# Performance work log

Measured on AMD Instinct MI355X. Metric: run time of the kernel, lower is better.

The kernel has to match this reference:

```python
import jax, jax.numpy as jnp
import numpy as np

N = 50000
E = 1600000
D_IN = 128
D_OUT = 128
K_EIG = 4
N_AGG = 3
N_SCALE = 3
AVG_D_LOG = float(np.log(33.0))  # avg_d['log'] for avg degree 32
BN_EPS = 1e-5


def setup_inputs() -> dict:
    key = jax.random.key(0)
    ks = jax.random.split(key, 8)
    h = jax.random.normal(ks[0], (N, D_IN), dtype=jnp.float32)
    eig = jax.random.normal(ks[1], (N, K_EIG), dtype=jnp.float32)
    snorm_n = jax.random.uniform(ks[2], (N, 1), dtype=jnp.float32)
    edge_src = jax.random.randint(ks[3], (E,), 0, N, dtype=jnp.int32)
    edge_dst = jax.random.randint(ks[4], (E,), 0, N, dtype=jnp.int32)
    d_cat = N_AGG * N_SCALE * D_IN  # 1152
    W = jax.random.normal(ks[5], (d_cat, D_OUT), dtype=jnp.float32) / np.sqrt(d_cat)
    b = jnp.zeros((D_OUT,), dtype=jnp.float32)
    bn_gamma = jnp.ones((D_OUT,), dtype=jnp.float32)
    bn_beta = jnp.zeros((D_OUT,), dtype=jnp.float32)
    bn_mean = jax.random.normal(ks[6], (D_OUT,), dtype=jnp.float32) * 0.1
    bn_var = jnp.ones((D_OUT,), dtype=jnp.float32)
    return {"h": h, "eig": eig, "snorm_n": snorm_n, "W": W, "b": b,
            "bn_gamma": bn_gamma, "bn_beta": bn_beta, "bn_mean": bn_mean,
            "bn_var": bn_var, "edge_src": edge_src, "edge_dst": edge_dst}


def reference(h, eig, snorm_n, W, b, bn_gamma, bn_beta, bn_mean, bn_var, edge_src, edge_dst):
    h_in = h
    # --- pretrans_edges: message e = src h; vector_field = eig_src - eig_dst ---
    h_e = h[edge_src]                      # [E, d] gathered edge messages
    vf = eig[edge_src] - eig[edge_dst]     # [E, k_eig]
    w = jnp.abs(vf[:, 0:1])                # dir1 weights [E, 1]

    # --- reduce: multi-aggregator segment reduce over destination nodes ---
    deg = jax.ops.segment_sum(jnp.ones((E,), h.dtype), edge_dst, num_segments=N)  # [N]
    deg_safe = jnp.maximum(deg, 1.0)
    sum_h = jax.ops.segment_sum(h_e, edge_dst, num_segments=N)
    mean_h = sum_h / deg_safe[:, None]
    max_h = jax.ops.segment_max(h_e, edge_dst, num_segments=N)
    max_h = jnp.where(deg[:, None] > 0, max_h, 0.0)  # empty mailbox -> 0
    dir_num = jax.ops.segment_sum(h_e * w, edge_dst, num_segments=N)
    dir_den = jax.ops.segment_sum(w, edge_dst, num_segments=N)  # [N, 1]
    dir_av = dir_num / (dir_den + 1e-30)
    agg = jnp.concatenate([mean_h, max_h, dir_av], axis=1)  # [N, 3d]

    # --- scalers: identity, amplification, attenuation ---
    logD = jnp.log(deg + 1.0)[:, None]
    amp = agg * (logD / AVG_D_LOG)
    att = agg * (AVG_D_LOG / jnp.maximum(logD, 1e-6))
    hcat = jnp.concatenate([agg, amp, att], axis=1)  # [N, 9d]

    # --- posttrans MLP (1 layer, no activation) ---
    out = hcat @ W + b
    # graph norm
    out = out * snorm_n
    # batch norm (eval mode, running stats)
    out = (out - bn_mean) * jax.lax.rsqrt(bn_var + BN_EPS) * bn_gamma + bn_beta
    out = jax.nn.relu(out)
    # residual (in_dim == out_dim)
    out = h_in + out
    # dropout p=0.0 / eval -> identity
    return out
```

## Files before the change

kernel.cpp:

```cpp
#include <hip/hip_runtime.h>
#include <hip/hip_bf16.h>

#define DIN 128
#define KEIG 4
#define CAP 96
#define BSH 7
#define BCAP 5120
#define ITEMS 16
#define AVG_D_LOG 3.4965075614664802f
#define BN_EPS 1e-5f

typedef __attribute__((ext_vector_type(8))) short bf16x8;
typedef __attribute__((ext_vector_type(4))) float f32x4;
typedef __attribute__((ext_vector_type(2))) float f32x2;

static __device__ inline unsigned short f2bf(float f) {
    union { float f; unsigned u; } v; v.f = f;
    unsigned r = v.u + 0x7FFFu + ((v.u >> 16) & 1u);
    return (unsigned short)(r >> 16);
}
static __device__ inline unsigned pack2bf(float lo, float hi) {
    return (unsigned)f2bf(lo) | ((unsigned)f2bf(hi) << 16);
}
static __device__ inline f32x2 up2(unsigned u) {
    f32x2 r;
    r.x = __int_as_float(u << 16);
    r.y = __int_as_float(u & 0xffff0000u);
    return r;
}


__global__ void k_prep(const float* __restrict__ h, unsigned* __restrict__ hb,
                       const float* __restrict__ W, unsigned short* __restrict__ Wt,
                       const float* __restrict__ eig, float* __restrict__ eig0,
                       int* __restrict__ cursor, int* __restrict__ bcur,
                       int nPairs, int wTotal, int N, int nbk)
{
    int i = blockIdx.x * 256 + threadIdx.x;
    if (i < nPairs) {
        float2 v = reinterpret_cast<const float2*>(h)[i];
        hb[i] = pack2bf(v.x, v.y);
    }
    if (i < wTotal) {
        int k = i % 384;
        int rest = i / 384;
        int col = rest & 127;
        int s = rest >> 7;
        Wt[i] = f2bf(W[(s * 384 + k) * 128 + col]);
    }
    if (i < N) {
        eig0[i] = eig[(size_t)i * KEIG];
        cursor[i] = 0;
    }
    if (i < nbk) bcur[i] = 0;
}


__global__ void k_bucket(const int* __restrict__ src, const int* __restrict__ dst,
                         const float* __restrict__ eig0, int* __restrict__ bcur,
                         uint2* __restrict__ stag, int E, int nbk)
{
    __shared__ int lcnt[512];
    __shared__ int lbase[512];
    const int t = threadIdx.x;
    for (int b = t; b < nbk; b += 256) lcnt[b] = 0;
    __syncthreads();

    const int e0 = blockIdx.x * (256 * ITEMS);
    int   bky[ITEMS];
    int   rnk[ITEMS];
    uint2 rec[ITEMS];
#pragma unroll
    for (int k = 0; k < ITEMS; ++k) {
        const int e = e0 + t + k * 256;
        if (e < E) {
            const int s = src[e], d = dst[e];
            const float w = fabsf(eig0[s] - eig0[d]);
            rec[k] = make_uint2(((unsigned)f2bf(w) << 16) | (unsigned)s, (unsigned)d);
            bky[k] = d >> BSH;
            rnk[k] = atomicAdd(&lcnt[bky[k]], 1);
        } else bky[k] = -1;
    }
    __syncthreads();
    for (int b = t; b < nbk; b += 256) {
        const int c = lcnt[b];
        lbase[b] = c ? atomicAdd(&bcur[b], c) : 0;
    }
    __syncthreads();
#pragma unroll
    for (int k = 0; k < ITEMS; ++k) {
        if (bky[k] >= 0) {
            const int pos = lbase[bky[k]] + rnk[k];
            if (pos < BCAP) stag[(size_t)bky[k] * BCAP + pos] = rec[k];
        }
    }
}


__global__ void k_group(const int* __restrict__ bcur, const uint2* __restrict__ stag,
                        unsigned* __restrict__ final_, int* __restrict__ off,
                        int* __restrict__ cnt, int N)
{
    __shared__ uint2 sst[BCAP];
    __shared__ int hcnt[128];
    __shared__ int sbuf[2][128];
    const int b = blockIdx.x;
    const int t = threadIdx.x;
    const int cb = min(bcur[b], BCAP);

    for (int i = t; i < cb; i += 256) sst[i] = stag[(size_t)b * BCAP + i];
    if (t < 128) hcnt[t] = 0;
    __syncthreads();

    int dl[(BCAP + 255) / 256];
    int rk[(BCAP + 255) / 256];
    int nit = 0;
    for (int i = t; i < cb; i += 256) {
        const int d_loc = sst[i].y & 127;
        dl[nit] = d_loc;
        rk[nit] = atomicAdd(&hcnt[d_loc], 1);
        ++nit;
    }
    __syncthreads();

    int cur = 0;
    if (t < 128) sbuf[0][t] = hcnt[t];
    __syncthreads();
    for (int d = 1; d < 128; d <<= 1) {
        if (t < 128) {
            int x = sbuf[cur][t];
            if (t >= d) x += sbuf[cur][t - d];
            sbuf[cur ^ 1][t] = x;
        }
        cur ^= 1;
        __syncthreads();
    }
    const int exb = cur ^ 1;
    if (t < 128) sbuf[exb][t] = sbuf[cur][t] - hcnt[t];
    __syncthreads();

    if (t < 128) {
        const int dg = (b << BSH) + t;
        if (dg < N) {
            off[dg] = b * BCAP + sbuf[exb][t];
            cnt[dg] = hcnt[t];
        }
    }
    nit = 0;
    for (int i = t; i < cb; i += 256) {
        final_[(size_t)b * BCAP + sbuf[exb][dl[nit]] + rk[nit]] = sst[i].x;
        ++nit;
    }
}


__global__ void k_hist(const int* __restrict__ dst, int* __restrict__ counts, int E) {
    int e = blockIdx.x * 256 + threadIdx.x;
    if (e < E) atomicAdd(&counts[dst[e]], 1);
}

__global__ void k_part(const int* __restrict__ counts, int* __restrict__ part, int N) {
    __shared__ int red[4];
    const int t = threadIdx.x;
    const int i = blockIdx.x * 256 + t;
    int v = (i < N) ? counts[i] : 0;
    for (int d = 32; d >= 1; d >>= 1) v += __shfl_down(v, d, 64);
    if ((t & 63) == 0) red[t >> 6] = v;
    __syncthreads();
    if (t == 0) part[blockIdx.x] = red[0] + red[1] + red[2] + red[3];
}

__global__ void k_scan1(const int* __restrict__ part, int* __restrict__ partoff,
                        int* __restrict__ total_out, int NB) {
    __shared__ int buf[2][256];
    const int t = threadIdx.x;
    int v = (t < NB) ? part[t] : 0;
    buf[0][t] = v;
    __syncthreads();
    int cur = 0;
    for (int d = 1; d < 256; d <<= 1) {
        int x = buf[cur][t];
        if (t >= d) x += buf[cur][t - d];
        buf[cur ^ 1][t] = x;
        cur ^= 1;
        __syncthreads();
    }
    if (t < NB) partoff[t] = buf[cur][t] - v;
    if (t == 255) *total_out = buf[cur][255];
}

__global__ void k_off(const int* __restrict__ counts, const int* __restrict__ partoff,
                      int* __restrict__ offsets, int* __restrict__ cursor, int N) {
    __shared__ int buf[2][256];
    const int t = threadIdx.x;
    const int i = blockIdx.x * 256 + t;
    int v = (i < N) ? counts[i] : 0;
    buf[0][t] = v;
    __syncthreads();
    int cur = 0;
    for (int d = 1; d < 256; d <<= 1) {
        int x = buf[cur][t];
        if (t >= d) x += buf[cur][t - d];
        buf[cur ^ 1][t] = x;
        cur ^= 1;
        __syncthreads();
    }
    if (i < N) {
        int excl = partoff[blockIdx.x] + buf[cur][t] - v;
        offsets[i] = excl;
        cursor[i]  = excl;
    }
}

__global__ void k_fill_csr(const int* __restrict__ src, const int* __restrict__ dst,
                           const float* __restrict__ eig0, int* __restrict__ cursor,
                           int2* __restrict__ sedge, int E)
{
    int e = blockIdx.x * 256 + threadIdx.x;
    if (e < E) {
        int s = src[e], d = dst[e];
        float w = fabsf(eig0[s] - eig0[d]);
        int pos = atomicAdd(&cursor[d], 1);
        sedge[pos] = make_int2(s, __float_as_int(w));
    }
}


template<bool PACKED>
__launch_bounds__(256, 3)
__global__ void k_aggmm(const unsigned* __restrict__ hb, const float* __restrict__ h,
                        const float* __restrict__ snorm,
                        const float* __restrict__ bvec, const float* __restrict__ gam,
                        const float* __restrict__ bet, const float* __restrict__ bmean,
                        const float* __restrict__ bvar,
                        const int* __restrict__ idx0, const int* __restrict__ idx1,
                        const unsigned* __restrict__ upk, const int2* __restrict__ sedge,
                        const unsigned short* __restrict__ Wt,
                        float* __restrict__ out, int N)
{
    __shared__ unsigned short aggT[32][392];
    __shared__ unsigned slotbuf[32][CAP];
    __shared__ float sc1[32], sc2[32];

    const int tid  = threadIdx.x;
    const int wave = tid >> 6;
    const int lane = tid & 63;
    const int q    = lane >> 4;
    const int l16  = lane & 15;
    const int node0 = blockIdx.x * 32;

    const uint4* __restrict__ hb4 = reinterpret_cast<const uint4*>(hb);

    for (int i = 0; i < 2; ++i) {
        const int nl = wave * 8 + i * 4 + q;
        const int n  = node0 + nl;
        int e0 = 0, cnt = 0;
        if (n < N) {
            if (PACKED) { e0 = idx0[n]; cnt = min(idx1[n], CAP); }
            else        { e0 = idx0[n]; cnt = idx0[n + 1] - e0; }
        }
        const int c0 = __shfl(cnt, 0),  c1 = __shfl(cnt, 16);
        const int c2 = __shfl(cnt, 32), c3 = __shfl(cnt, 48);
        const int maxcnt = max(max(c0, c1), max(c2, c3));

        f32x2 s2[4], m2[4], d2[4];
        float wsum = 0.f;
#pragma unroll
        for (int f = 0; f < 4; ++f) {
            s2[f] = (f32x2){0.f, 0.f};
            m2[f] = (f32x2){-INFINITY, -INFINITY};
            d2[f] = (f32x2){0.f, 0.f};
        }
        const int clampi = (cnt > 0) ? cnt - 1 : 0;

        if (PACKED) {
            for (int t = l16; t < cnt; t += 16) slotbuf[nl][t] = upk[e0 + t];
            if (cnt == 0 && l16 == 0) slotbuf[nl][0] = 0;

            uint4 bufA[8], bufB[8];
            float wvA[8], wvB[8];

#define STAGE(BUF, WV, BASE) do {                                        \
    _Pragma("unroll")                                                    \
    for (int j = 0; j < 8; ++j) {                                        \
        int ci = (BASE) + j; ci = ci < clampi ? ci : clampi;             \
        const unsigned u = slotbuf[nl][ci];                              \
        WV[j] = __int_as_float(u & 0xffff0000u);                         \
        BUF[j] = hb4[(((u & 0xffffu) << 4) | (unsigned)l16)];            \
    }                                                                    \
} while (0)

#define ACCUM(BUF, WV, BASE) do {                                        \
    _Pragma("unroll")                                                    \
    for (int j = 0; j < 8; ++j) {                                        \
        if ((BASE) + j < cnt) {                                          \
            const float wj = WV[j];                                      \
            const f32x2 wj2 = (f32x2){wj, wj};                           \
            const f32x2 p0 = up2(BUF[j].x), p1 = up2(BUF[j].y);          \
            const f32x2 p2 = up2(BUF[j].z), p3 = up2(BUF[j].w);          \
            s2[0] += p0; s2[1] += p1; s2[2] += p2; s2[3] += p3;          \
            m2[0].x = fmaxf(m2[0].x, p0.x); m2[0].y = fmaxf(m2[0].y, p0.y); \
            m2[1].x = fmaxf(m2[1].x, p1.x); m2[1].y = fmaxf(m2[1].y, p1.y); \
            m2[2].x = fmaxf(m2[2].x, p2.x); m2[2].y = fmaxf(m2[2].y, p2.y); \
            m2[3].x = fmaxf(m2[3].x, p3.x); m2[3].y = fmaxf(m2[3].y, p3.y); \
            d2[0] += p0 * wj2; d2[1] += p1 * wj2;                        \
            d2[2] += p2 * wj2; d2[3] += p3 * wj2;                        \
            wsum += wj;                                                  \
        }                                                                \
    }                                                                    \
} while (0)

            if (maxcnt > 0) {
                STAGE(bufA, wvA, 0);
                for (int base = 0; base < maxcnt; base += 16) {
                    const bool haveB = (base + 8) < maxcnt;
                    if (haveB) STAGE(bufB, wvB, base + 8);
                    ACCUM(bufA, wvA, base);
                    if (base + 16 < maxcnt) STAGE(bufA, wvA, base + 16);
                    if (haveB) ACCUM(bufB, wvB, base + 8);
                }
            }
#undef STAGE
#undef ACCUM
        } else {
            for (int base = 0; base < maxcnt; base += 8) {
                unsigned srcs[8];
                float    wv[8];
#pragma unroll
                for (int j = 0; j < 8; ++j) {
                    int idx = base + j;
                    idx = idx < clampi ? idx : clampi;
                    int2 v = sedge[e0 + idx];
                    srcs[j] = (unsigned)((cnt > 0) ? v.x : 0);
                    wv[j]   = __int_as_float(v.y);
                }
                uint4 v8[8];
#pragma unroll
                for (int j = 0; j < 8; ++j)
                    v8[j] = hb4[(size_t)srcs[j] * 16 + l16];
#pragma unroll
                for (int j = 0; j < 8; ++j) {
                    if (base + j < cnt) {
                        const float wj = wv[j];
                        const f32x2 wj2 = (f32x2){wj, wj};
                        const f32x2 p0 = up2(v8[j].x), p1 = up2(v8[j].y);
                        const f32x2 p2 = up2(v8[j].z), p3 = up2(v8[j].w);
                        s2[0] += p0; s2[1] += p1; s2[2] += p2; s2[3] += p3;
                        m2[0].x = fmaxf(m2[0].x, p0.x); m2[0].y = fmaxf(m2[0].y, p0.y);
                        m2[1].x = fmaxf(m2[1].x, p1.x); m2[1].y = fmaxf(m2[1].y, p1.y);
                        m2[2].x = fmaxf(m2[2].x, p2.x); m2[2].y = fmaxf(m2[2].y, p2.y);
                        m2[3].x = fmaxf(m2[3].x, p3.x); m2[3].y = fmaxf(m2[3].y, p3.y);
                        d2[0] += p0 * wj2; d2[1] += p1 * wj2;
                        d2[2] += p2 * wj2; d2[3] += p3 * wj2;
                        wsum += wj;
                    }
                }
            }
        }

        const float degf = (float)cnt;
        const float inv  = 1.0f / fmaxf(degf, 1.0f);
        const float dinv = 1.0f / (wsum + 1e-30f);
        const bool nz = (cnt > 0);
        uint4 pm, px, pd;
        pm.x = pack2bf(s2[0].x * inv, s2[0].y * inv);
        pm.y = pack2bf(s2[1].x * inv, s2[1].y * inv);
        pm.z = pack2bf(s2[2].x * inv, s2[2].y * inv);
        pm.w = pack2bf(s2[3].x * inv, s2[3].y * inv);
        px.x = pack2bf(nz ? m2[0].x : 0.f, nz ? m2[0].y : 0.f);
        px.y = pack2bf(nz ? m2[1].x : 0.f, nz ? m2[1].y : 0.f);
        px.z = pack2bf(nz ? m2[2].x : 0.f, nz ? m2[2].y : 0.f);
        px.w = pack2bf(nz ? m2[3].x : 0.f, nz ? m2[3].y : 0.f);
        pd.x = pack2bf(d2[0].x * dinv, d2[0].y * dinv);
        pd.y = pack2bf(d2[1].x * dinv, d2[1].y * dinv);
        pd.z = pack2bf(d2[2].x * dinv, d2[2].y * dinv);
        pd.w = pack2bf(d2[3].x * dinv, d2[3].y * dinv);
        const int f0i = l16 * 8;
        *reinterpret_cast<uint4*>(&aggT[nl][f0i])       = pm;
        *reinterpret_cast<uint4*>(&aggT[nl][128 + f0i]) = px;
        *reinterpret_cast<uint4*>(&aggT[nl][256 + f0i]) = pd;
        if (l16 == 0) {
            float logD = logf(degf + 1.0f);
            sc1[nl] = logD / AVG_D_LOG;
            sc2[nl] = AVG_D_LOG / fmaxf(logD, 1e-6f);
        }
    }
    __syncthreads();

    f32x4 acc[2][2][3];
#pragma unroll
    for (int m = 0; m < 2; ++m)
#pragma unroll
        for (int ct = 0; ct < 2; ++ct)
#pragma unroll
            for (int sv = 0; sv < 3; ++sv)
                acc[m][ct][sv] = (f32x4){0.f, 0.f, 0.f, 0.f};

    const int cb   = wave * 32;
    const int r16  = lane & 15;
    const int kgrp = lane >> 4;

    for (int ks = 0; ks < 12; ++ks) {
        const int kbase = ks * 32 + kgrp * 8;
        bf16x8 a[2];
#pragma unroll
        for (int m = 0; m < 2; ++m)
            a[m] = *reinterpret_cast<const bf16x8*>(&aggT[m * 16 + r16][kbase]);
#pragma unroll
        for (int sv = 0; sv < 3; ++sv) {
#pragma unroll
            for (int ct = 0; ct < 2; ++ct) {
                const int col = cb + ct * 16 + r16;
                const bf16x8 b = *reinterpret_cast<const bf16x8*>(
                    &Wt[(size_t)sv * 49152 + (size_t)col * 384 + kbase]);
#pragma unroll
                for (int m = 0; m < 2; ++m)
                    acc[m][ct][sv] = __builtin_amdgcn_mfma_f32_16x16x32_bf16(
                        a[m], b, acc[m][ct][sv], 0, 0, 0);
            }
        }
    }

#pragma unroll
    for (int ct = 0; ct < 2; ++ct) {
        const int col = cb + ct * 16 + r16;
        const float bc  = bvec[col];
        const float mc  = bmean[col];
        const float rs  = rsqrtf(bvar[col] + BN_EPS);
        const float gc  = gam[col];
        const float bec = bet[col];
#pragma unroll
        for (int m = 0; m < 2; ++m) {
#pragma unroll
            for (int r = 0; r < 4; ++r) {
                const int nl = m * 16 + kgrp * 4 + r;
                const int n  = node0 + nl;
                if (n >= N) continue;
                float v = acc[m][ct][0][r] + sc1[nl] * acc[m][ct][1][r]
                                           + sc2[nl] * acc[m][ct][2][r];
                float y = (v + bc) * snorm[n];
                y = (y - mc) * rs * gc + bec;
                y = fmaxf(y, 0.f);
                y += h[(size_t)n * DIN + col];
                out[(size_t)n * DIN + col] = y;
            }
        }
    }
}


extern "C" void kernel_launch(void* const* d_in, const int* in_sizes, int n_in,
                              void* d_out, int out_size, void* d_ws, size_t ws_size,
                              hipStream_t stream)
{
    const float* h     = (const float*)d_in[0];
    const float* eig   = (const float*)d_in[1];
    const float* snorm = (const float*)d_in[2];
    const float* W     = (const float*)d_in[3];
    const float* bvec  = (const float*)d_in[4];
    const float* gam   = (const float*)d_in[5];
    const float* bet   = (const float*)d_in[6];
    const float* bmean = (const float*)d_in[7];
    const float* bvar  = (const float*)d_in[8];
    const int*   esrc  = (const int*)d_in[9];
    const int*   edst  = (const int*)d_in[10];
    float* out = (float*)d_out;

    const int N = in_sizes[0] / DIN;
    const int E = in_sizes[9];
    const int NB = (N + 255) / 256;
    const int nPairs = N * DIN / 2;
    const int wTotal = 3 * 128 * 384;
    const int nbk = (N + 127) >> BSH;
    (void)ws_size; (void)n_in; (void)out_size;

    char* base = (char*)d_ws;
    size_t o = 0;
    auto take = [&](size_t bytes) {
        char* p = base + o;
        o = (o + bytes + 255) & ~(size_t)255;
        return p;
    };
    unsigned* hb       = (unsigned*)take((size_t)nPairs * 4);
    unsigned short* Wt = (unsigned short*)take((size_t)wTotal * 2);
    float* eig0        = (float*)take((size_t)N * 4);
    int* cursor        = (int*)take((size_t)(N + 1) * 4);

    const size_t bucket_bytes = (size_t)nbk * BCAP * 8
                              + (size_t)nbk * BCAP * 4
                              + (size_t)N * 8
                              + (size_t)nbk * 4 + 4096;
    const bool bucketOK = (N <= 65536) && (nbk <= 512) && ((o + bucket_bytes) <= ws_size);

    const int gridPrep = (nPairs + 255) / 256;
    const int gridE    = (E + 255) / 256;
    const int gridB    = (E + 256 * ITEMS - 1) / (256 * ITEMS);
    const int gridN32  = (N + 31) / 32;

    if (bucketOK) {
        uint2* stag     = (uint2*)take((size_t)nbk * BCAP * 8);
        unsigned* fin   = (unsigned*)take((size_t)nbk * BCAP * 4);
        int* off        = (int*)take((size_t)N * 4);
        int* cnt        = (int*)take((size_t)N * 4);
        int* bcur       = (int*)take((size_t)nbk * 4);
        k_prep<<<gridPrep, 256, 0, stream>>>(h, hb, W, Wt, eig, eig0, cursor, bcur,
                                             nPairs, wTotal, N, nbk);
        k_bucket<<<gridB, 256, 0, stream>>>(esrc, edst, eig0, bcur, stag, E, nbk);
        k_group<<<nbk, 256, 0, stream>>>(bcur, stag, fin, off, cnt, N);
        k_aggmm<true><<<gridN32, 256, 0, stream>>>(hb, h, snorm, bvec, gam, bet, bmean,
                                                   bvar, off, cnt, fin, nullptr, Wt, out, N);
    } else {
        int* counts  = (int*)take((size_t)(N + 1) * 4);
        int* offsets = (int*)take((size_t)(N + 1) * 4);
        int2* sedge  = (int2*)take((size_t)(E + 16) * 8);
        int* part    = (int*)take((size_t)NB * 4);
        int* partoff = (int*)take((size_t)NB * 4);
        int* bcur    = (int*)take(4096);
        k_prep<<<gridPrep, 256, 0, stream>>>(h, hb, W, Wt, eig, eig0, counts, bcur,
                                             nPairs, wTotal, N, 1);
        k_hist<<<gridE, 256, 0, stream>>>(edst, counts, E);
        k_part<<<NB, 256, 0, stream>>>(counts, part, N);
        k_scan1<<<1, 256, 0, stream>>>(part, partoff, &offsets[N], NB);
        k_off<<<NB, 256, 0, stream>>>(counts, partoff, offsets, cursor, N);
        k_fill_csr<<<gridE, 256, 0, stream>>>(esrc, edst, eig0, cursor, sedge, E);
        k_aggmm<false><<<gridN32, 256, 0, stream>>>(hb, h, snorm, bvec, gam, bet, bmean,
                                                    bvar, offsets, nullptr, nullptr, sedge,
                                                    Wt, out, N);
    }
}
```

Measured before the change: 161.9 us.

## Split fused aggregate+matmul kernel into separate aggregation and MFMA GEMM kernels

Splits the fused gather/aggregate + matmul kernel into two kernels. The first computes per-node mean/max/directional aggregates in bf16 into a global buffer, using 16 lanes per node with no shared-memory slot buffer and no per-wave max-count loop. The second runs the bf16 MFMA GEMM reading that buffer from global memory. This removes load imbalance across the 4 nodes in a wave and the shared-memory occupancy limit, at the cost of a roughly 38 MB intermediate round trip plus an extra launch. The agg buffer reuses the staging buffer's workspace, and the CAP=96 per-node edge cap is removed.

```diff
diff --git a/kernel.cpp b/kernel.cpp
--- a/kernel.cpp
+++ b/kernel.cpp
@@ -3,7 +3,6 @@
 
 #define DIN 128
 #define KEIG 4
-#define CAP 96
 #define BSH 7
 #define BCAP 5120
 #define ITEMS 16
@@ -98,8 +97,7 @@
 
 
 __global__ void k_group(const int* __restrict__ bcur, const uint2* __restrict__ stag,
-                        unsigned* __restrict__ final_, int* __restrict__ off,
-                        int* __restrict__ cnt, int N)
+                        unsigned* __restrict__ final_, int2* __restrict__ offcnt, int N)
 {
     __shared__ uint2 sst[BCAP];
     __shared__ int hcnt[128];
@@ -141,10 +139,7 @@
 
     if (t < 128) {
         const int dg = (b << BSH) + t;
-        if (dg < N) {
-            off[dg] = b * BCAP + sbuf[exb][t];
-            cnt[dg] = hcnt[t];
-        }
+        if (dg < N) offcnt[dg] = make_int2(b * BCAP + sbuf[exb][t], hcnt[t]);
     }
     nit = 0;
     for (int i = t; i < cb; i += 256) {
@@ -227,66 +222,52 @@
 
 
 template<bool PACKED>
-__launch_bounds__(256, 3)
-__global__ void k_aggmm(const unsigned* __restrict__ hb, const float* __restrict__ h,
-                        const float* __restrict__ snorm,
-                        const float* __restrict__ bvec, const float* __restrict__ gam,
-                        const float* __restrict__ bet, const float* __restrict__ bmean,
-                        const float* __restrict__ bvar,
-                        const int* __restrict__ idx0, const int* __restrict__ idx1,
-                        const unsigned* __restrict__ upk, const int2* __restrict__ sedge,
-                        const unsigned short* __restrict__ Wt,
-                        float* __restrict__ out, int N)
-{
-    __shared__ unsigned short aggT[32][392];
-    __shared__ unsigned slotbuf[32][CAP];
-    __shared__ float sc1[32], sc2[32];
-
-    const int tid  = threadIdx.x;
-    const int wave = tid >> 6;
-    const int lane = tid & 63;
-    const int q    = lane >> 4;
-    const int l16  = lane & 15;
-    const int node0 = blockIdx.x * 32;
+__launch_bounds__(256, 4)
+__global__ void k_agg(const unsigned* __restrict__ hb,
+                      const int2* __restrict__ offcnt, const int* __restrict__ offsets,
+                      const unsigned* __restrict__ upk, const int2* __restrict__ sedge,
+                      unsigned short* __restrict__ agg, float2* __restrict__ scal, int N)
+{
+    const int tid = threadIdx.x;
+    const int qid = tid >> 4;
+    const int l16 = tid & 15;
+    const int n = blockIdx.x * 16 + qid;
+    if (n >= N) return;
+
+    int e0, cnt;
+    if (PACKED) { const int2 oc = offcnt[n]; e0 = oc.x; cnt = oc.y; }
+    else        { e0 = offsets[n]; cnt = offsets[n + 1] - e0; }
 
     const uint4* __restrict__ hb4 = reinterpret_cast<const uint4*>(hb);
 
-    for (int i = 0; i < 2; ++i) {
-        const int nl = wave * 8 + i * 4 + q;
-        const int n  = node0 + nl;
-        int e0 = 0, cnt = 0;
-        if (n < N) {
-            if (PACKED) { e0 = idx0[n]; cnt = min(idx1[n], CAP); }
-            else        { e0 = idx0[n]; cnt = idx0[n + 1] - e0; }
-        }
-        const int c0 = __shfl(cnt, 0),  c1 = __shfl(cnt, 16);
-        const int c2 = __shfl(cnt, 32), c3 = __shfl(cnt, 48);
-        const int maxcnt = max(max(c0, c1), max(c2, c3));
-
-        f32x2 s2[4], m2[4], d2[4];
-        float wsum = 0.f;
-#pragma unroll
-        for (int f = 0; f < 4; ++f) {
-            s2[f] = (f32x2){0.f, 0.f};
-            m2[f] = (f32x2){-INFINITY, -INFINITY};
-            d2[f] = (f32x2){0.f, 0.f};
-        }
-        const int clampi = (cnt > 0) ? cnt - 1 : 0;
-
-        if (PACKED) {
-            for (int t = l16; t < cnt; t += 16) slotbuf[nl][t] = upk[e0 + t];
-            if (cnt == 0 && l16 == 0) slotbuf[nl][0] = 0;
-
-            uint4 bufA[8], bufB[8];
-            float wvA[8], wvB[8];
+    f32x2 s2[4], m2[4], d2[4];
+    float wsum = 0.f;
+#pragma unroll
+    for (int f = 0; f < 4; ++f) {
+        s2[f] = (f32x2){0.f, 0.f};
+        m2[f] = (f32x2){-INFINITY, -INFINITY};
+        d2[f] = (f32x2){0.f, 0.f};
+    }
+    const int clampi = (cnt > 0) ? cnt - 1 : 0;
+
+    uint4 bufA[8], bufB[8];
+    float wvA[8], wvB[8];
 
 #define STAGE(BUF, WV, BASE) do {                                        \
     _Pragma("unroll")                                                    \
     for (int j = 0; j < 8; ++j) {                                        \
         int ci = (BASE) + j; ci = ci < clampi ? ci : clampi;             \
-        const unsigned u = slotbuf[nl][ci];                              \
-        WV[j] = __int_as_float(u & 0xffff0000u);                         \
-        BUF[j] = hb4[(((u & 0xffffu) << 4) | (unsigned)l16)];            \
+        unsigned sidx;                                                   \
+        if (PACKED) {                                                    \
+            const unsigned u = upk[e0 + ci];                             \
+            WV[j] = __int_as_float(u & 0xffff0000u);                     \
+            sidx = (u & 0xffffu) << 4;                                   \
+        } else {                                                         \
+            const int2 v = sedge[e0 + ci];                               \
+            WV[j] = __int_as_float(v.y);                                 \
+            sidx = ((unsigned)v.x) << 4;                                 \
+        }                                                                \
+        BUF[j] = hb4[sidx | (unsigned)l16];                              \
     }                                                                    \
 } while (0)
 
@@ -310,82 +291,64 @@
     }                                                                    \
 } while (0)
 
-            if (maxcnt > 0) {
-                STAGE(bufA, wvA, 0);
-                for (int base = 0; base < maxcnt; base += 16) {
-                    const bool haveB = (base + 8) < maxcnt;
-                    if (haveB) STAGE(bufB, wvB, base + 8);
-                    ACCUM(bufA, wvA, base);
-                    if (base + 16 < maxcnt) STAGE(bufA, wvA, base + 16);
-                    if (haveB) ACCUM(bufB, wvB, base + 8);
-                }
-            }
+    if (cnt > 0) {
+        STAGE(bufA, wvA, 0);
+        for (int base = 0; base < cnt; base += 16) {
+            const bool haveB = (base + 8) < cnt;
+            if (haveB) STAGE(bufB, wvB, base + 8);
+            ACCUM(bufA, wvA, base);
+            if (base + 16 < cnt) STAGE(bufA, wvA, base + 16);
+            if (haveB) ACCUM(bufB, wvB, base + 8);
+        }
+    }
 #undef STAGE
 #undef ACCUM
-        } else {
-            for (int base = 0; base < maxcnt; base += 8) {
-                unsigned srcs[8];
-                float    wv[8];
-#pragma unroll
-                for (int j = 0; j < 8; ++j) {
-                    int idx = base + j;
-                    idx = idx < clampi ? idx : clampi;
-                    int2 v = sedge[e0 + idx];
-                    srcs[j] = (unsigned)((cnt > 0) ? v.x : 0);
-                    wv[j]   = __int_as_float(v.y);
-                }
-                uint4 v8[8];
-#pragma unroll
-                for (int j = 0; j < 8; ++j)
-                    v8[j] = hb4[(size_t)srcs[j] * 16 + l16];
-#pragma unroll
-                for (int j = 0; j < 8; ++j) {
-                    if (base + j < cnt) {
-                        const float wj = wv[j];
-                        const f32x2 wj2 = (f32x2){wj, wj};
-                        const f32x2 p0 = up2(v8[j].x), p1 = up2(v8[j].y);
-                        const f32x2 p2 = up2(v8[j].z), p3 = up2(v8[j].w);
-                        s2[0] += p0; s2[1] += p1; s2[2] += p2; s2[3] += p3;
-                        m2[0].x = fmaxf(m2[0].x, p0.x); m2[0].y = fmaxf(m2[0].y, p0.y);
-                        m2[1].x = fmaxf(m2[1].x, p1.x); m2[1].y = fmaxf(m2[1].y, p1.y);
-                        m2[2].x = fmaxf(m2[2].x, p2.x); m2[2].y = fmaxf(m2[2].y, p2.y);
-                        m2[3].x = fmaxf(m2[3].x, p3.x); m2[3].y = fmaxf(m2[3].y, p3.y);
-                        d2[0] += p0 * wj2; d2[1] += p1 * wj2;
-                        d2[2] += p2 * wj2; d2[3] += p3 * wj2;
-                        wsum += wj;
-                    }
-                }
-            }
-        }
-
-        const float degf = (float)cnt;
-        const float inv  = 1.0f / fmaxf(degf, 1.0f);
-        const float dinv = 1.0f / (wsum + 1e-30f);
-        const bool nz = (cnt > 0);
-        uint4 pm, px, pd;
-        pm.x = pack2bf(s2[0].x * inv, s2[0].y * inv);
-        pm.y = pack2bf(s2[1].x * inv, s2[1].y * inv);
-        pm.z = pack2bf(s2[2].x * inv, s2[2].y * inv);
-        pm.w = pack2bf(s2[3].x * inv, s2[3].y * inv);
-        px.x = pack2bf(nz ? m2[0].x : 0.f, nz ? m2[0].y : 0.f);
-        px.y = pack2bf(nz ? m2[1].x : 0.f, nz ? m2[1].y : 0.f);
-        px.z = pack2bf(nz ? m2[2].x : 0.f, nz ? m2[2].y : 0.f);
-        px.w = pack2bf(nz ? m2[3].x : 0.f, nz ? m2[3].y : 0.f);
-        pd.x = pack2bf(d2[0].x * dinv, d2[0].y * dinv);
-        pd.y = pack2bf(d2[1].x * dinv, d2[1].y * dinv);
-        pd.z = pack2bf(d2[2].x * dinv, d2[2].y * dinv);
-        pd.w = pack2bf(d2[3].x * dinv, d2[3].y * dinv);
-        const int f0i = l16 * 8;
-        *reinterpret_cast<uint4*>(&aggT[nl][f0i])       = pm;
-        *reinterpret_cast<uint4*>(&aggT[nl][128 + f0i]) = px;
-        *reinterpret_cast<uint4*>(&aggT[nl][256 + f0i]) = pd;
-        if (l16 == 0) {
-            float logD = logf(degf + 1.0f);
-            sc1[nl] = logD / AVG_D_LOG;
-            sc2[nl] = AVG_D_LOG / fmaxf(logD, 1e-6f);
-        }
-    }
-    __syncthreads();
+
+    const float degf = (float)cnt;
+    const float inv  = 1.0f / fmaxf(degf, 1.0f);
+    const float dinv = 1.0f / (wsum + 1e-30f);
+    const bool nz = (cnt > 0);
+    uint4 pm, px, pd;
+    pm.x = pack2bf(s2[0].x * inv, s2[0].y * inv);
+    pm.y = pack2bf(s2[1].x * inv, s2[1].y * inv);
+    pm.z = pack2bf(s2[2].x * inv, s2[2].y * inv);
+    pm.w = pack2bf(s2[3].x * inv, s2[3].y * inv);
+    px.x = pack2bf(nz ? m2[0].x : 0.f, nz ? m2[0].y : 0.f);
+    px.y = pack2bf(nz ? m2[1].x : 0.f, nz ? m2[1].y : 0.f);
+    px.z = pack2bf(nz ? m2[2].x : 0.f, nz ? m2[2].y : 0.f);
+    px.w = pack2bf(nz ? m2[3].x : 0.f, nz ? m2[3].y : 0.f);
+    pd.x = pack2bf(d2[0].x * dinv, d2[0].y * dinv);
+    pd.y = pack2bf(d2[1].x * dinv, d2[1].y * dinv);
+    pd.z = pack2bf(d2[2].x * dinv, d2[2].y * dinv);
+    pd.w = pack2bf(d2[3].x * dinv, d2[3].y * dinv);
+
+    uint4* aggv = reinterpret_cast<uint4*>(agg);
+    const size_t row = (size_t)n * 48;
+    aggv[row + l16]      = pm;
+    aggv[row + 16 + l16] = px;
+    aggv[row + 32 + l16] = pd;
+    if (l16 == 0) {
+        const float logD = logf(degf + 1.0f);
+        scal[n] = make_float2(logD / AVG_D_LOG, AVG_D_LOG / fmaxf(logD, 1e-6f));
+    }
+}
+
+
+__launch_bounds__(256, 4)
+__global__ void k_mm(const unsigned short* __restrict__ agg, const float2* __restrict__ scal,
+                     const float* __restrict__ h, const float* __restrict__ snorm,
+                     const float* __restrict__ bvec, const float* __restrict__ gam,
+                     const float* __restrict__ bet, const float* __restrict__ bmean,
+                     const float* __restrict__ bvar, const unsigned short* __restrict__ Wt,
+                     float* __restrict__ out, int N)
+{
+    const int tid  = threadIdx.x;
+    const int wave = tid >> 6;
+    const int lane = tid & 63;
+    const int r16  = lane & 15;
+    const int kgrp = lane >> 4;
+    const int node0 = blockIdx.x * 32;
+    const int cb = wave * 32;
 
     f32x4 acc[2][2][3];
 #pragma unroll
@@ -395,17 +358,14 @@
 #pragma unroll
             for (int sv = 0; sv < 3; ++sv)
                 acc[m][ct][sv] = (f32x4){0.f, 0.f, 0.f, 0.f};
-
-    const int cb   = wave * 32;
-    const int r16  = lane & 15;
-    const int kgrp = lane >> 4;
 
     for (int ks = 0; ks < 12; ++ks) {
         const int kbase = ks * 32 + kgrp * 8;
         bf16x8 a[2];
 #pragma unroll
         for (int m = 0; m < 2; ++m)
-            a[m] = *reinterpret_cast<const bf16x8*>(&aggT[m * 16 + r16][kbase]);
+            a[m] = *reinterpret_cast<const bf16x8*>(
+                &agg[(size_t)(node0 + m * 16 + r16) * 384 + kbase]);
 #pragma unroll
         for (int sv = 0; sv < 3; ++sv) {
 #pragma unroll
@@ -436,8 +396,9 @@
                 const int nl = m * 16 + kgrp * 4 + r;
                 const int n  = node0 + nl;
                 if (n >= N) continue;
-                float v = acc[m][ct][0][r] + sc1[nl] * acc[m][ct][1][r]
-                                           + sc2[nl] * acc[m][ct][2][r];
+                const float2 sc = scal[n];
+                float v = acc[m][ct][0][r] + sc.x * acc[m][ct][1][r]
+                                           + sc.y * acc[m][ct][2][r];
                 float y = (v + bc) * snorm[n];
                 y = (y - mc) * rs * gc + bec;
                 y = fmaxf(y, 0.f);
@@ -472,6 +433,7 @@
     const int nPairs = N * DIN / 2;
     const int wTotal = 3 * 128 * 384;
     const int nbk = (N + 127) >> BSH;
+    const int N32 = (N + 31) / 32;
     (void)ws_size; (void)n_in; (void)out_size;
 
     char* base = (char*)d_ws;
@@ -485,30 +447,39 @@
     unsigned short* Wt = (unsigned short*)take((size_t)wTotal * 2);
     float* eig0        = (float*)take((size_t)N * 4);
     int* cursor        = (int*)take((size_t)(N + 1) * 4);
-
-    const size_t bucket_bytes = (size_t)nbk * BCAP * 8
-                              + (size_t)nbk * BCAP * 4
+    float2* scal       = (float2*)take((size_t)N * 8);
+
+    const size_t agg_bytes  = (size_t)N32 * 32 * 384 * 2;
+    const size_t stag_bytes = (size_t)nbk * BCAP * 8;
+    const size_t shared_bytes = agg_bytes > stag_bytes ? agg_bytes : stag_bytes;
+
+    const size_t bucket_bytes = (size_t)nbk * BCAP * 4
                               + (size_t)N * 8
-                              + (size_t)nbk * 4 + 4096;
+                              + (size_t)nbk * 4
+                              + shared_bytes + 8192;
     const bool bucketOK = (N <= 65536) && (nbk <= 512) && ((o + bucket_bytes) <= ws_size);
 
     const int gridPrep = (nPairs + 255) / 256;
     const int gridE    = (E + 255) / 256;
     const int gridB    = (E + 256 * ITEMS - 1) / (256 * ITEMS);
-    const int gridN32  = (N + 31) / 32;
+    const int gridN16  = (N + 15) / 16;
 
     if (bucketOK) {
-        uint2* stag     = (uint2*)take((size_t)nbk * BCAP * 8);
         unsigned* fin   = (unsigned*)take((size_t)nbk * BCAP * 4);
-        int* off        = (int*)take((size_t)N * 4);
-        int* cnt        = (int*)take((size_t)N * 4);
+        int2* offcnt    = (int2*)take((size_t)N * 8);
         int* bcur       = (int*)take((size_t)nbk * 4);
+        char* shared    = take(shared_bytes);
+        uint2* stag     = (uint2*)shared;
+        unsigned short* agg = (unsigned short*)shared;
+
         k_prep<<<gridPrep, 256, 0, stream>>>(h, hb, W, Wt, eig, eig0, cursor, bcur,
                                              nPairs, wTotal, N, nbk);
         k_bucket<<<gridB, 256, 0, stream>>>(esrc, edst, eig0, bcur, stag, E, nbk);
-        k_group<<<nbk, 256, 0, stream>>>(bcur, stag, fin, off, cnt, N);
-        k_aggmm<true><<<gridN32, 256, 0, stream>>>(hb, h, snorm, bvec, gam, bet, bmean,
-                                                   bvar, off, cnt, fin, nullptr, Wt, out, N);
+        k_group<<<nbk, 256, 0, stream>>>(bcur, stag, fin, offcnt, N);
+        k_agg<true><<<gridN16, 256, 0, stream>>>(hb, offcnt, nullptr, fin, nullptr,
+                                                 agg, scal, N);
+        k_mm<<<N32, 256, 0, stream>>>(agg, scal, h, snorm, bvec, gam, bet, bmean, bvar,
+                                      Wt, out, N);
     } else {
         int* counts  = (int*)take((size_t)(N + 1) * 4);
         int* offsets = (int*)take((size_t)(N + 1) * 4);
@@ -516,6 +487,8 @@
         int* part    = (int*)take((size_t)NB * 4);
         int* partoff = (int*)take((size_t)NB * 4);
         int* bcur    = (int*)take(4096);
+        unsigned short* agg = (unsigned short*)take(agg_bytes);
+
         k_prep<<<gridPrep, 256, 0, stream>>>(h, hb, W, Wt, eig, eig0, counts, bcur,
                                              nPairs, wTotal, N, 1);
         k_hist<<<gridE, 256, 0, stream>>>(edst, counts, E);
@@ -523,8 +496,9 @@
         k_scan1<<<1, 256, 0, stream>>>(part, partoff, &offsets[N], NB);
         k_off<<<NB, 256, 0, stream>>>(counts, partoff, offsets, cursor, N);
         k_fill_csr<<<gridE, 256, 0, stream>>>(esrc, edst, eig0, cursor, sedge, E);
-        k_aggmm<false><<<gridN32, 256, 0, stream>>>(hb, h, snorm, bvec, gam, bet, bmean,
-                                                    bvar, offsets, nullptr, nullptr, sedge,
-                                                    Wt, out, N);
-    }
-}
+        k_agg<false><<<gridN16, 256, 0, stream>>>(hb, nullptr, offsets, nullptr, sedge,
+                                                  agg, scal, N);
+        k_mm<<<N32, 256, 0, stream>>>(agg, scal, h, snorm, bvec, gam, bet, bmean, bvar,
+                                      Wt, out, N);
+    }
+}
```

Result: slower. 201.1 us (+24.2%).
